# Kernel tuning notes

Hardware: AMD Instinct MI355X
Metric: run time of the kernel (lower is better)

Reference implementation:

```python
import jax, jax.numpy as jnp
import numpy as np

# ---- constants from init_kwargs ----
PC = (-51.2, -51.2, -5.0, 51.2, 51.2, 3.0)
D = 4          # num_points_in_pillar
ZMAX = 8       # Z default in gen_reference_points
BEV_H = 256; BEV_W = 256
Q = BEV_H * BEV_W
NUMCAM = 6
VBH = 256; VBW = 256
MAXLEN = VBH * VBW
MAX_OVER = 6
IMH, IMW = 512, 928   # data['img'].shape[2:]
EPS = 1e-5


def _gen_ref3d(bs):
    # gen_reference_points(dim='3d'): (bs, D, Q, 3), normalized coords
    zs = jnp.linspace(0.5, ZMAX - 0.5, D) / ZMAX
    xs = jnp.linspace(0.5, BEV_W - 0.5, BEV_W) / BEV_W
    ys = jnp.linspace(0.5, BEV_H - 0.5, BEV_H) / BEV_H
    g = jnp.stack([
        jnp.broadcast_to(xs[None, None, :], (D, BEV_H, BEV_W)),
        jnp.broadcast_to(ys[None, :, None], (D, BEV_H, BEV_W)),
        jnp.broadcast_to(zs[:, None, None], (D, BEV_H, BEV_W)),
    ], -1).reshape(D, Q, 3)
    return jnp.broadcast_to(g[None], (bs, D, Q, 3))


def setup_inputs() -> dict:
    key = jax.random.key(0)
    ego2img = jax.random.normal(key, (4, NUMCAM, 4, 4), dtype=jnp.float32)
    return {"ego2img": ego2img}


def reference(ego2img):
    B = ego2img.shape[0]
    ref = _gen_ref3d(B)                                   # (B,D,Q,3)
    x = ref[..., 0] * (PC[3] - PC[0]) + PC[0]
    y = ref[..., 1] * (PC[4] - PC[1]) + PC[1]
    z = ref[..., 2] * (PC[5] - PC[2]) + PC[2]
    pts = jnp.stack([x, y, z, jnp.ones_like(x)], -1)      # (B,D,Q,4) homogeneous

    # project each pillar point through each camera matrix
    cam = jnp.einsum('bcij,bdqj->bcdqi', ego2img, pts)    # (B,C,D,Q,4)
    zc = cam[..., 2]
    uv = cam[..., 0:2] / jnp.maximum(zc, EPS)[..., None]
    u = uv[..., 0] / IMW
    v = uv[..., 1] / IMH
    vis = (zc > EPS) & (v > 0.0) & (v < 1.0) & (u < 1.0) & (u > 0.0)  # (B,C,D,Q)
    rpc = jnp.clip(jnp.stack([u, v], -1), -2.1, 2.1)       # (B,C,D,Q,2)

    ref_cam = jnp.transpose(rpc, (1, 0, 3, 2, 4))          # (C,B,Q,D,2)
    vis_any = jnp.any(jnp.transpose(vis, (1, 0, 3, 2)), -1)  # (C,B,Q) pillar visible in cam

    qidx = jnp.arange(Q)
    qx = qidx % BEV_W
    qy = qidx // BEV_W
    # normalized BEV coords of each pillar (align_corners=True convention)
    gxy = jnp.stack([qx / (BEV_W - 1.0), qy / (BEV_H - 1.0)], -1) * 2.0 - 1.0

    # ---- queries_rebatch_grid: pack visible pillar coords densely per camera ----
    vis_bc = jnp.transpose(vis_any, (1, 0, 2)).reshape(B * NUMCAM, Q)

    def make_grid(vrow):
        rank = jnp.cumsum(vrow.astype(jnp.int32)) - 1      # position among visible pillars
        pos = jnp.where(vrow, rank, MAXLEN)                # invisible -> dummy slot
        buf = jnp.full((MAXLEN + 1, 2), -1.5, dtype=jnp.float32)
        return buf.at[pos].set(gxy)[:MAXLEN]

    grids = jax.vmap(make_grid)(vis_bc)                    # (B*C, MAXLEN, 2)
    queries_rebatch_grid = grids.reshape(B * NUMCAM, VBH, VBW, 2)

    # ---- reference_points_rebatch: grid_sample(nearest, align_corners=True, zeros pad) ----
    src = jnp.transpose(ref_cam.reshape(NUMCAM, B, Q, D * 2), (1, 0, 3, 2))
    src = src.reshape(B * NUMCAM, D * 2, Q)               # (B*C, D*2, H*W)
    ix = jnp.round((grids[..., 0] + 1.0) * 0.5 * (BEV_W - 1)).astype(jnp.int32)
    iy = jnp.round((grids[..., 1] + 1.0) * 0.5 * (BEV_H - 1)).astype(jnp.int32)
    ok = (ix >= 0) & (ix < BEV_W) & (iy >= 0) & (iy < BEV_H)
    gq = jnp.clip(iy * BEV_W + ix, 0, Q - 1)              # (B*C, MAXLEN)
    gathered = jnp.take_along_axis(src, gq[:, None, :], axis=2) * ok[:, None, :]
    reference_points_rebatch = jnp.transpose(gathered, (0, 2, 1)).reshape(
        B * NUMCAM, MAXLEN, D, 2)

    # ---- restore_bev_grid: map each (camera, pillar) slot back to dense BEV rows ----
    RB = MAX_OVER * BEV_H * BEV_W
    cam_off = jnp.arange(NUMCAM)[:, None] * VBH

    def make_restore(vis_b):  # (C, Q) bool
        vi = vis_b.astype(jnp.int32)
        rank = jnp.cumsum(vi, axis=1) - 1                  # packed index inside camera
        over = jnp.cumsum(vi, axis=0) - vi                 # overlap slot (exclusive count)
        gx = (rank % VBW) / (VBW - 1.0) * 2.0 - 1.0
        gy = (cam_off + rank // VBW) / (NUMCAM * VBH - 1.0) * 2.0 - 1.0
        flat = (over * BEV_H + qy[None]) * BEV_W + qx[None]
        flat = jnp.where(vis_b & (over < MAX_OVER), flat, RB)
        buf = jnp.full((RB + 1, 2), -1.5, dtype=jnp.float32)
        buf = buf.at[flat.reshape(-1)].set(jnp.stack([gx, gy], -1).reshape(-1, 2))
        return buf[:RB].reshape(MAX_OVER * BEV_H, BEV_W, 2)

    restore_bev_grid = jax.vmap(make_restore)(jnp.transpose(vis_any, (1, 0, 2)))

    # ---- bev_pillar_counts: 1 / (#cameras seeing each pillar) ----
    count = jnp.sum(vis_any.astype(jnp.float32), axis=0)   # (B, Q)
    bev_pillar_counts = (1.0 / jnp.maximum(count, 1.0))[..., None]

    return (queries_rebatch_grid, restore_bev_grid,
            reference_points_rebatch, bev_pillar_counts)
```

## Files before the change

### kernel.cpp

```cpp
#include <hip/hip_runtime.h>

#define NCAM      6
#define NB        4
#define NROWS     24
#define NQ        65536
#define MAXLEN_   65536

#define OFF_QGRID   0
#define OFF_RESTORE 3145728
#define OFF_REFPTS  6291456
#define OFF_COUNTS  18874368

__device__ __forceinline__ float zval(int d) {
    const float z[4] = { -4.5f, -2.16666674613952637f,
                          0.166666507720947266f, 2.5f };
    return z[d];
}

__device__ __forceinline__ float clip21(float x) {
    return fminf(fmaxf(x, -2.1f), 2.1f);
}

__device__ __forceinline__ bool proj_point(const float m[12], float x, float y, float z,
                                           float& u, float& v) {
    float c0 = ((m[0]*x + m[1]*y) + m[2]*z) + m[3];
    float c1 = ((m[4]*x + m[5]*y) + m[6]*z) + m[7];
    float c2 = ((m[8]*x + m[9]*y) + m[10]*z) + m[11];
    float zcl = fmaxf(c2, 1e-5f);
    u = (c0 / zcl) / 928.0f;
    v = (c1 / zcl) / 512.0f;
    return (c2 > 1e-5f) & (v > 0.0f) & (v < 1.0f) & (u < 1.0f) & (u > 0.0f);
}

__device__ __forceinline__ void load_mat(const float* __restrict__ ego2img, int row, float m[12]) {
    const float* M = ego2img + row * 16;
    #pragma unroll
    for (int i = 0; i < 12; ++i) m[i] = M[i];
}

__device__ __forceinline__ void bev_xy(int qx, int qy, float& x, float& y) {
    x = ((float)qx + 0.5f) * (1.0f/256.0f) * 102.4f - 51.2f;
    y = ((float)qy + 0.5f) * (1.0f/256.0f) * 102.4f - 51.2f;
}

__global__ void __launch_bounds__(256)
k_count(const float* __restrict__ ego2img, int* __restrict__ chunkCounts)
{
    int chunk = blockIdx.x, row = blockIdx.y;
    float m[12]; load_mat(ego2img, row, m);
    int t = threadIdx.x;
    int q0 = chunk * 1024 + t * 4;
    int cnt = 0;
    #pragma unroll
    for (int i = 0; i < 4; ++i) {
        int q = q0 + i;
        float x, y; bev_xy(q & 255, q >> 8, x, y);
        bool va = false;
        #pragma unroll
        for (int d = 0; d < 4; ++d) {
            float u, v;
            va |= proj_point(m, x, y, zval(d), u, v);
        }
        cnt += va ? 1 : 0;
    }
    #pragma unroll
    for (int off = 32; off > 0; off >>= 1) cnt += __shfl_down(cnt, off, 64);
    if ((t & 63) == 0)
        chunkCounts[row * 256 + chunk * 4 + (t >> 6)] = cnt;
}

__global__ void __launch_bounds__(256)
k_fused(const float* __restrict__ ego2img, const int* __restrict__ chunkCounts,
        float* __restrict__ out)
{
    int chunk = blockIdx.x, b = blockIdx.y;
    int t = threadIdx.x;
    int lane = t & 63, wid = t >> 6;

    __shared__ int sBase[NCAM], sTotal[NCAM];
    __shared__ int waveIncl[NCAM][4];
    __shared__ int ranks[NCAM][256];

    for (int c = wid; c < NCAM; c += 4) {
        const int* p = chunkCounts + (b * NCAM + c) * 256;
        int4 v4 = ((const int4*)p)[lane];
        int s = v4.x + v4.y + v4.z + v4.w;
        int incl = s;
        #pragma unroll
        for (int off = 1; off < 64; off <<= 1) {
            int n = __shfl_up(incl, off, 64);
            if (lane >= off) incl += n;
        }
        if (lane == (chunk >> 2)) {
            int base = incl - s;
            int k = chunk & 3;
            if (k > 0) base += v4.x;
            if (k > 1) base += v4.y;
            if (k > 2) base += v4.z;
            sBase[c] = base;
        }
        if (lane == 63) sTotal[c] = incl;
    }

    int q  = chunk * 256 + t;
    int qx = t, qy = chunk;
    float x, y; bev_xy(qx, qy, x, y);

    for (int c = 0; c < NCAM; ++c) {
        float m[12]; load_mat(ego2img, b * NCAM + c, m);
        float uv[8];
        bool vis = false;
        #pragma unroll
        for (int d = 0; d < 4; ++d) {
            float u, v;
            bool vi = proj_point(m, x, y, zval(d), u, v);
            uv[2*d]   = clip21(u);
            uv[2*d+1] = clip21(v);
            vis |= vi;
        }
        int cnt = vis ? 1 : 0;
        int incl = cnt;
        #pragma unroll
        for (int off = 1; off < 64; off <<= 1) {
            int n = __shfl_up(incl, off, 64);
            if (lane >= off) incl += n;
        }
        if (lane == 63) waveIncl[c][wid] = incl;
        __syncthreads();
        int base = sBase[c];
        #pragma unroll
        for (int w = 0; w < 3; ++w) if (w < wid) base += waveIncl[c][w];
        int r = base + incl - cnt;

        float2* qgrid = (float2*)(out + OFF_QGRID)  + (size_t)(b * NCAM + c) * MAXLEN_;
        float4* refp  = (float4*)(out + OFF_REFPTS) + (size_t)(b * NCAM + c) * MAXLEN_ * 2;

        if (vis) {
            float2 g;
            g.x = ((float)qx / 255.0f) * 2.0f - 1.0f;
            g.y = ((float)qy / 255.0f) * 2.0f - 1.0f;
            qgrid[r] = g;
            refp[2*r]   = make_float4(uv[0], uv[1], uv[2], uv[3]);
            refp[2*r+1] = make_float4(uv[4], uv[5], uv[6], uv[7]);
            ranks[c][t] = r;
        } else {
            ranks[c][t] = -1;
        }
        if (q >= sTotal[c]) {
            qgrid[q] = make_float2(-1.5f, -1.5f);
            float4 z4 = make_float4(0.f, 0.f, 0.f, 0.f);
            refp[2*q]   = z4;
            refp[2*q+1] = z4;
        }
    }
    __syncthreads();

    float2* rest = (float2*)(out + OFF_RESTORE) + (size_t)b * NCAM * NQ;
    int over = 0;
    #pragma unroll
    for (int c = 0; c < NCAM; ++c) {
        int r = ranks[c][t];
        if (r >= 0) {
            float gx = ((float)(r & 255) / 255.0f) * 2.0f - 1.0f;
            float gy = ((float)(c * 256 + (r >> 8)) / 1535.0f) * 2.0f - 1.0f;
            rest[(over * 256 + qy) * 256 + qx] = make_float2(gx, gy);
            ++over;
        }
    }
    for (int o = over; o < NCAM; ++o)
        rest[(o * 256 + qy) * 256 + qx] = make_float2(-1.5f, -1.5f);
    out[OFF_COUNTS + b * NQ + q] = 1.0f / fmaxf((float)over, 1.0f);
}

extern "C" void kernel_launch(void* const* d_in, const int* in_sizes, int n_in,
                              void* d_out, int out_size, void* d_ws, size_t ws_size,
                              hipStream_t stream)
{
    const float* ego2img = (const float*)d_in[0];
    float* out = (float*)d_out;
    int* chunkCounts = (int*)d_ws;

    k_count<<<dim3(64, NROWS), 256, 0, stream>>>(ego2img, chunkCounts);
    k_fused<<<dim3(256, NB),   256, 0, stream>>>(ego2img, chunkCounts, out);
}
```

Baseline: 99.43 us.

## Merge count and scatter kernels into one cooperative kernel with grid sync

Replaces the separate counting kernel with a first phase inside a single cooperative kernel. Each block counts visible pillars per camera for its own BEV row with a ballot, writes them to workspace, and a grid-wide sync separates this from the prefix and scatter phase. This removes one kernel launch and the launch gap between the two kernels. In exchange it adds grid-sync overhead and requires all 1024 blocks to be co-resident, which occupancy bounds of 4 blocks per CU must allow.

```diff
diff --git a/kernel.cpp b/kernel.cpp
--- a/kernel.cpp
+++ b/kernel.cpp
@@ -1,4 +1,7 @@
 #include <hip/hip_runtime.h>
+#include <hip/hip_cooperative_groups.h>
+
+namespace cg = cooperative_groups;
 
 #define NCAM      6
 #define NB        4
@@ -43,46 +46,42 @@
     y = ((float)qy + 0.5f) * (1.0f/256.0f) * 102.4f - 51.2f;
 }
 
-__global__ void __launch_bounds__(256)
-k_count(const float* __restrict__ ego2img, int* __restrict__ chunkCounts)
-{
-    int chunk = blockIdx.x, row = blockIdx.y;
-    float m[12]; load_mat(ego2img, row, m);
-    int t = threadIdx.x;
-    int q0 = chunk * 1024 + t * 4;
-    int cnt = 0;
-    #pragma unroll
-    for (int i = 0; i < 4; ++i) {
-        int q = q0 + i;
-        float x, y; bev_xy(q & 255, q >> 8, x, y);
-        bool va = false;
-        #pragma unroll
-        for (int d = 0; d < 4; ++d) {
-            float u, v;
-            va |= proj_point(m, x, y, zval(d), u, v);
-        }
-        cnt += va ? 1 : 0;
-    }
-    #pragma unroll
-    for (int off = 32; off > 0; off >>= 1) cnt += __shfl_down(cnt, off, 64);
-    if ((t & 63) == 0)
-        chunkCounts[row * 256 + chunk * 4 + (t >> 6)] = cnt;
-}
-
-__global__ void __launch_bounds__(256)
-k_fused(const float* __restrict__ ego2img, const int* __restrict__ chunkCounts,
-        float* __restrict__ out)
+__global__ void __launch_bounds__(256, 4)
+k_all(const float* __restrict__ ego2img, int* __restrict__ counts,
+      float* __restrict__ out)
 {
     int chunk = blockIdx.x, b = blockIdx.y;
     int t = threadIdx.x;
     int lane = t & 63, wid = t >> 6;
+    int qx = t, qy = chunk;
+    int q = chunk * 256 + t;
+    float x, y; bev_xy(qx, qy, x, y);
 
+    __shared__ int wcnt[NCAM][4];
     __shared__ int sBase[NCAM], sTotal[NCAM];
     __shared__ int waveIncl[NCAM][4];
     __shared__ int ranks[NCAM][256];
 
+    for (int c = 0; c < NCAM; ++c) {
+        float m[12]; load_mat(ego2img, b * NCAM + c, m);
+        bool vis = false;
+        #pragma unroll
+        for (int d = 0; d < 4; ++d) {
+            float u, v;
+            vis |= proj_point(m, x, y, zval(d), u, v);
+        }
+        unsigned long long bal = __ballot(vis);
+        if (lane == 0) wcnt[c][wid] = __popcll(bal);
+    }
+    __syncthreads();
+    if (t < NCAM)
+        counts[(b * NCAM + t) * 256 + chunk] =
+            wcnt[t][0] + wcnt[t][1] + wcnt[t][2] + wcnt[t][3];
+
+    cg::this_grid().sync();
+
     for (int c = wid; c < NCAM; c += 4) {
-        const int* p = chunkCounts + (b * NCAM + c) * 256;
+        const int* p = counts + (b * NCAM + c) * 256;
         int4 v4 = ((const int4*)p)[lane];
         int s = v4.x + v4.y + v4.z + v4.w;
         int incl = s;
@@ -101,10 +100,6 @@
         }
         if (lane == 63) sTotal[c] = incl;
     }
-
-    int q  = chunk * 256 + t;
-    int qx = t, qy = chunk;
-    float x, y; bev_xy(qx, qy, x, y);
 
     for (int c = 0; c < NCAM; ++c) {
         float m[12]; load_mat(ego2img, b * NCAM + c, m);
@@ -178,8 +173,9 @@
 {
     const float* ego2img = (const float*)d_in[0];
     float* out = (float*)d_out;
-    int* chunkCounts = (int*)d_ws;
+    int* counts = (int*)d_ws;
 
-    k_count<<<dim3(64, NROWS), 256, 0, stream>>>(ego2img, chunkCounts);
-    k_fused<<<dim3(256, NB),   256, 0, stream>>>(ego2img, chunkCounts, out);
+    void* args[] = { (void*)&ego2img, (void*)&counts, (void*)&out };
+    hipLaunchCooperativeKernel((const void*)k_all, dim3(256, NB), dim3(256, 1, 1),
+                               args, 0, stream);
 }
```

Result: slower. 173.0 us (+74.0%).
